# Optimization experiments

Measured on AMD Instinct MI355X. Metric: run time of the kernel, lower is better.

Reference implementation:

```python
import jax, jax.numpy as jnp
import numpy as np

D_MODEL = 1024
NUM_HEADS = 16
D_HEAD = D_MODEL // NUM_HEADS


def setup_inputs() -> dict:
    key = jax.random.key(0)
    ks = jax.random.split(key, 11)
    B, S = 2, 2048
    s = 1.0 / np.sqrt(D_MODEL)
    inp = {
        "Q": jax.random.normal(ks[0], (B, S, D_MODEL), dtype=jnp.float32),
        "K": jax.random.normal(ks[1], (B, S, D_MODEL), dtype=jnp.float32),
        "V": jax.random.normal(ks[2], (B, S, D_MODEL), dtype=jnp.float32),
        "W_q": jax.random.normal(ks[3], (D_MODEL, D_MODEL), dtype=jnp.float32) * s,
        "b_q": jnp.zeros((D_MODEL,), dtype=jnp.float32),
        "W_k": jax.random.normal(ks[4], (D_MODEL, D_MODEL), dtype=jnp.float32) * s,
        "b_k": jnp.zeros((D_MODEL,), dtype=jnp.float32),
        "W_v": jax.random.normal(ks[5], (D_MODEL, D_MODEL), dtype=jnp.float32) * s,
        "b_v": jnp.zeros((D_MODEL,), dtype=jnp.float32),
        "W_o": jax.random.normal(ks[6], (D_MODEL, D_MODEL), dtype=jnp.float32) * s,
        "b_o": jnp.zeros((D_MODEL,), dtype=jnp.float32),
    }
    return inp


def reference(Q, K, V, W_q, b_q, W_k, b_k, W_v, b_v, W_o, b_o):
    B, S, _ = Q.shape
    # Linear projections (torch Linear: x @ W.T + b)
    q = Q @ W_q.T + b_q  # [B,S,D]
    k = K @ W_k.T + b_k
    v = V @ W_v.T + b_v
    # split heads -> [B,H,S,d]
    q = q.reshape(B, S, NUM_HEADS, D_HEAD).transpose(0, 2, 1, 3)
    k = k.reshape(B, S, NUM_HEADS, D_HEAD).transpose(0, 2, 1, 3)
    v = v.reshape(B, S, NUM_HEADS, D_HEAD).transpose(0, 2, 1, 3)
    scores = jnp.einsum("bhqd,bhkd->bhqk", q, k) / np.sqrt(D_HEAD).astype(np.float32)
    attn = jax.nn.softmax(scores, axis=-1)
    out = jnp.einsum("bhqk,bhkd->bhqd", attn, v)
    out = out.transpose(0, 2, 1, 3).reshape(B, S, D_MODEL)
    return out @ W_o.T + b_o
```

## Files before the change

### kernel.cpp

```cpp
#include <hip/hip_runtime.h>
#include <stdint.h>

#define D_MODEL 1024
#define S_LEN   2048
#define BATCH   2
#define NHEAD   16
#define DHEAD   64
#define NTOK    (BATCH * S_LEN)

typedef unsigned short u16;
typedef __attribute__((ext_vector_type(8))) short bf16x8;
typedef __attribute__((ext_vector_type(4))) float f32x4;
typedef __attribute__((ext_vector_type(16))) float f32x16;
typedef __attribute__((ext_vector_type(2))) unsigned int u32x2;

__device__ __forceinline__ unsigned pack2bf(float lo, float hi) {
    unsigned a = __float_as_uint(lo) + 0x8000u;
    unsigned b = __float_as_uint(hi) + 0x8000u;
    return __builtin_amdgcn_perm(b, a, 0x07060302u);
}
__device__ __forceinline__ u16 f2bf1(float f) {
    return (u16)((__float_as_uint(f) + 0x8000u) >> 16);
}

#define GAS(p) ((const __attribute__((address_space(1))) void*)(p))
#define LAS(p) ((__attribute__((address_space(3))) void*)(p))
#define SWZ8(row, c) (((((row) << 3) | ((c) ^ ((row) & 7)))) << 3)

__global__ __launch_bounds__(256) void convert_kernel(
    const float* __restrict__ Q, const float* __restrict__ K, const float* __restrict__ V,
    const float* __restrict__ Wq, const float* __restrict__ Wk,
    const float* __restrict__ Wv, const float* __restrict__ Wo,
    u16* __restrict__ Qb, u16* __restrict__ Kb, u16* __restrict__ Vb,
    u16* __restrict__ Wqb, u16* __restrict__ Wkb, u16* __restrict__ Wvb, u16* __restrict__ Wob)
{
    const size_t SEG = 262144;
    size_t start = (size_t)blockIdx.x * 4096;
    int s = (int)(start / SEG);
    const float* src; u16* dst; size_t seg0;
    if (s < 4)       { src = Q;  dst = Qb;  seg0 = 0; }
    else if (s < 8)  { src = K;  dst = Kb;  seg0 = 4 * SEG; }
    else if (s < 12) { src = V;  dst = Vb;  seg0 = 8 * SEG; }
    else if (s == 12){ src = Wq; dst = Wqb; seg0 = 12 * SEG; }
    else if (s == 13){ src = Wk; dst = Wkb; seg0 = 13 * SEG; }
    else if (s == 14){ src = Wv; dst = Wvb; seg0 = 14 * SEG; }
    else             { src = Wo; dst = Wob; seg0 = 15 * SEG; }
    size_t off = start - seg0 + threadIdx.x;
    const float4* s4 = (const float4*)src;
    #pragma unroll
    for (int k = 0; k < 16; ++k) {
        float4 x = s4[off + (size_t)k * 256];
        u32x2 p = (u32x2){pack2bf(x.x, x.y), pack2bf(x.z, x.w)};
        *(u32x2*)(dst + (off + (size_t)k * 256) * 4) = p;
    }
}

__global__ __launch_bounds__(256) void proj_kernel(
    const u16* __restrict__ Qb, const u16* __restrict__ Kb, const u16* __restrict__ Vb,
    const u16* __restrict__ Wqb, const u16* __restrict__ Wkb, const u16* __restrict__ Wvb,
    const float* __restrict__ bq, const float* __restrict__ bk, const float* __restrict__ bv,
    u16* __restrict__ qw, u16* __restrict__ kw, u16* __restrict__ vtw)
{
    const int z = blockIdx.z;
    const int bx = blockIdx.x;
    const u16* A = (z == 0) ? Wqb : (z == 1) ? Wkb : Wvb;
    const u16* B = (z == 0) ? Qb  : (z == 1) ? Kb  : Vb;
    const float* bias = (z == 0) ? bq : (z == 1) ? bk : bv;
    const int mbase = (bx & 7) * 128;
    const int nbase = (bx >> 3) * 128;

    const int tid = threadIdx.x, lane = tid & 63, wave = tid >> 6;
    const int m16 = lane & 15, quad = lane >> 4;
    const int wm = wave >> 1, wn = wave & 1;

    __shared__ __align__(16) u16 As[128 * 64];
    __shared__ __align__(16) u16 Bs[128 * 64];

    int srow[4], scg[4];
    #pragma unroll
    for (int c = 0; c < 4; ++c) {
        int p = (wave * 4 + c) * 64 + lane;
        srow[c] = p >> 3;
        scg[c]  = (p & 7) ^ (srow[c] & 7);
    }

    f32x4 acc[4][4];
    #pragma unroll
    for (int mt = 0; mt < 4; ++mt)
        #pragma unroll
        for (int nt = 0; nt < 4; ++nt) acc[mt][nt] = (f32x4){0.f, 0.f, 0.f, 0.f};

    for (int kc = 0; kc < D_MODEL; kc += 64) {
        #pragma unroll
        for (int c = 0; c < 4; ++c) {
            __builtin_amdgcn_global_load_lds(
                GAS(A + (size_t)(mbase + srow[c]) * D_MODEL + kc + scg[c] * 8),
                LAS(As + (wave * 4 + c) * 512), 16, 0, 0);
            __builtin_amdgcn_global_load_lds(
                GAS(B + (size_t)(nbase + srow[c]) * D_MODEL + kc + scg[c] * 8),
                LAS(Bs + (wave * 4 + c) * 512), 16, 0, 0);
        }
        __syncthreads();
        #pragma unroll
        for (int half = 0; half < 2; ++half) {
            bf16x8 af[4], bfr[4];
            #pragma unroll
            for (int mt = 0; mt < 4; ++mt)
                af[mt] = *(const bf16x8*)&As[SWZ8(wm * 64 + mt * 16 + m16, quad + 4 * half)];
            #pragma unroll
            for (int nt = 0; nt < 4; ++nt)
                bfr[nt] = *(const bf16x8*)&Bs[SWZ8(wn * 64 + nt * 16 + m16, quad + 4 * half)];
            #pragma unroll
            for (int mt = 0; mt < 4; ++mt)
                #pragma unroll
                for (int nt = 0; nt < 4; ++nt)
                    acc[mt][nt] = __builtin_amdgcn_mfma_f32_16x16x32_bf16(af[mt], bfr[nt], acc[mt][nt], 0, 0, 0);
        }
        __syncthreads();
    }

    if (z < 2) {
        u16* Y = z ? kw : qw;
        const float scale = z ? 1.0f : 0.18033688011112042f;
        #pragma unroll
        for (int mt = 0; mt < 4; ++mt) {
            int d0 = mbase + wm * 64 + mt * 16 + quad * 4;
            float4 b4 = *(const float4*)&bias[d0];
            #pragma unroll
            for (int nt = 0; nt < 4; ++nt) {
                int tok = nbase + wn * 64 + nt * 16 + m16;
                float v0 = (acc[mt][nt][0] + b4.x) * scale;
                float v1 = (acc[mt][nt][1] + b4.y) * scale;
                float v2 = (acc[mt][nt][2] + b4.z) * scale;
                float v3 = (acc[mt][nt][3] + b4.w) * scale;
                *(u32x2*)(Y + (size_t)tok * D_MODEL + d0) =
                    (u32x2){pack2bf(v0, v1), pack2bf(v2, v3)};
            }
        }
    } else {
        #pragma unroll
        for (int mt = 0; mt < 4; ++mt)
            #pragma unroll
            for (int r = 0; r < 4; ++r) {
                int dout = mbase + wm * 64 + mt * 16 + quad * 4 + r;
                float bb = bias[dout];
                #pragma unroll
                for (int nt = 0; nt < 4; ++nt) {
                    int tok = nbase + wn * 64 + nt * 16 + m16;
                    vtw[(size_t)dout * NTOK + tok] = f2bf1(acc[mt][nt][r] + bb);
                }
            }
    }
}

__global__ __launch_bounds__(256, 2) void attn_kernel(
    const u16* __restrict__ qw, const u16* __restrict__ kw,
    const u16* __restrict__ vtw, u16* __restrict__ aw)
{
    const int qbase = blockIdx.x * 128;
    const int h = blockIdx.y, b = blockIdx.z;
    const int tid = threadIdx.x, lane = tid & 63, wave = tid >> 6;
    const int l31 = lane & 31;
    const int hh  = lane >> 5;
    const int colbase = h * DHEAD;
    const size_t qrow0 = (size_t)b * S_LEN + qbase;

    __shared__ __align__(16) u16 Ks[2][64 * 64];
    __shared__ __align__(16) u16 Vs[2][64 * 64];

    int srow[2], scg[2];
    #pragma unroll
    for (int i = 0; i < 2; ++i) {
        int p = (wave * 2 + i) * 64 + lane;
        srow[i] = p >> 3;
        scg[i]  = (p & 7) ^ (srow[i] & 7);
    }

    #define STAGE_KV(buf, kv0)                                                              \
        do {                                                                                \
            _Pragma("unroll")                                                               \
            for (int i_ = 0; i_ < 2; ++i_) {                                                \
                __builtin_amdgcn_global_load_lds(                                           \
                    GAS(kw + ((size_t)b * S_LEN + (kv0) + srow[i_]) * D_MODEL + colbase + scg[i_] * 8), \
                    LAS(Ks[buf] + (wave * 2 + i_) * 512), 16, 0, 0);                        \
                __builtin_amdgcn_global_load_lds(                                           \
                    GAS(vtw + (size_t)(colbase + srow[i_]) * NTOK + (size_t)b * S_LEN + (kv0) + scg[i_] * 8), \
                    LAS(Vs[buf] + (wave * 2 + i_) * 512), 16, 0, 0);                        \
            }                                                                               \
        } while (0)

    bf16x8 qf[4];
    {
        const u16* qptr = qw + (qrow0 + wave * 32 + l31) * D_MODEL + colbase + hh * 8;
        #pragma unroll
        for (int s = 0; s < 4; ++s) qf[s] = *(const bf16x8*)(qptr + s * 16);
    }

    STAGE_KV(0, 0);

    f32x16 o[2];
    #pragma unroll
    for (int dt = 0; dt < 2; ++dt)
        #pragma unroll
        for (int r = 0; r < 16; ++r) o[dt][r] = 0.f;
    float l = 0.f;

    __syncthreads();

    for (int t = 0; t < S_LEN / 64; ++t) {
        const int cur = t & 1;
        if (t + 1 < S_LEN / 64) STAGE_KV(!cur, (t + 1) * 64);

        f32x16 sc[2];
        #pragma unroll
        for (int kt = 0; kt < 2; ++kt) {
            #pragma unroll
            for (int r = 0; r < 16; ++r) sc[kt][r] = -12.f;
            #pragma unroll
            for (int s = 0; s < 4; ++s) {
                bf16x8 kf = *(const bf16x8*)&Ks[cur][SWZ8(kt * 32 + l31, s * 2 + hh)];
                sc[kt] = __builtin_amdgcn_mfma_f32_32x32x16_bf16(kf, qf[s], sc[kt], 0, 0, 0);
            }
        }

        unsigned x[2][4][2], y[2][4][2];
        #pragma unroll
        for (int kt = 0; kt < 2; ++kt)
            #pragma unroll
            for (int g = 0; g < 4; ++g) {
                float p0 = __builtin_amdgcn_exp2f(sc[kt][4 * g + 0]);
                float p1 = __builtin_amdgcn_exp2f(sc[kt][4 * g + 1]);
                float p2 = __builtin_amdgcn_exp2f(sc[kt][4 * g + 2]);
                float p3 = __builtin_amdgcn_exp2f(sc[kt][4 * g + 3]);
                l += (p0 + p1) + (p2 + p3);
                x[kt][g][0] = pack2bf(p0, p1);
                x[kt][g][1] = pack2bf(p2, p3);
            }
        #pragma unroll
        for (int kt = 0; kt < 2; ++kt)
            #pragma unroll
            for (int g = 0; g < 4; ++g) {
                y[kt][g][0] = __shfl_xor((int)x[kt][g][0], 32);
                y[kt][g][1] = __shfl_xor((int)x[kt][g][1], 32);
            }

        #pragma unroll
        for (int kt = 0; kt < 2; ++kt)
            #pragma unroll
            for (int sp = 0; sp < 2; ++sp) {
                int ge = 2 * sp, go = 2 * sp + 1;
                union { unsigned u[4]; bf16x8 v; } pf;
                pf.u[0] = hh ? y[kt][go][0] : x[kt][ge][0];
                pf.u[1] = hh ? y[kt][go][1] : x[kt][ge][1];
                pf.u[2] = hh ? x[kt][go][0] : y[kt][ge][0];
                pf.u[3] = hh ? x[kt][go][1] : y[kt][ge][1];
                #pragma unroll
                for (int dt = 0; dt < 2; ++dt) {
                    bf16x8 vf = *(const bf16x8*)&Vs[cur][SWZ8(dt * 32 + l31, (2 * kt + sp) * 2 + hh)];
                    o[dt] = __builtin_amdgcn_mfma_f32_32x32x16_bf16(vf, pf.v, o[dt], 0, 0, 0);
                }
            }

        __syncthreads();
    }

    l += __shfl_xor(l, 32);
    float inv = 1.0f / l;

    size_t orow = (qrow0 + wave * 32 + l31) * D_MODEL + colbase;
    #pragma unroll
    for (int dt = 0; dt < 2; ++dt)
        #pragma unroll
        for (int g = 0; g < 4; ++g) {
            float v0 = o[dt][4 * g + 0] * inv, v1 = o[dt][4 * g + 1] * inv;
            float v2 = o[dt][4 * g + 2] * inv, v3 = o[dt][4 * g + 3] * inv;
            *(u32x2*)(aw + orow + dt * 32 + 8 * g + 4 * hh) =
                (u32x2){pack2bf(v0, v1), pack2bf(v2, v3)};
        }
    #undef STAGE_KV
}

__global__ __launch_bounds__(256) void outproj_kernel(
    const u16* __restrict__ aw, const u16* __restrict__ Wob,
    const float* __restrict__ bo, float* __restrict__ out)
{
    const int nbase = blockIdx.x * 64;
    const int mbase = blockIdx.y * 128;
    const int tid = threadIdx.x, lane = tid & 63, wave = tid >> 6;
    const int m16 = lane & 15, quad = lane >> 4;
    const int wm = wave >> 1, wn = wave & 1;

    __shared__ __align__(16) u16 As[128 * 64];
    __shared__ __align__(16) u16 Bs[64 * 64];

    int arow[4], acg[4], brow[2], bcg[2];
    #pragma unroll
    for (int c = 0; c < 4; ++c) {
        int p = (wave * 4 + c) * 64 + lane;
        arow[c] = p >> 3; acg[c] = (p & 7) ^ (arow[c] & 7);
    }
    #pragma unroll
    for (int c = 0; c < 2; ++c) {
        int p = (wave * 2 + c) * 64 + lane;
        brow[c] = p >> 3; bcg[c] = (p & 7) ^ (brow[c] & 7);
    }

    f32x4 acc[4][2];
    #pragma unroll
    for (int mt = 0; mt < 4; ++mt)
        #pragma unroll
        for (int nt = 0; nt < 2; ++nt) acc[mt][nt] = (f32x4){0.f, 0.f, 0.f, 0.f};

    for (int kc = 0; kc < D_MODEL; kc += 64) {
        #pragma unroll
        for (int c = 0; c < 4; ++c)
            __builtin_amdgcn_global_load_lds(
                GAS(Wob + (size_t)(mbase + arow[c]) * D_MODEL + kc + acg[c] * 8),
                LAS(As + (wave * 4 + c) * 512), 16, 0, 0);
        #pragma unroll
        for (int c = 0; c < 2; ++c)
            __builtin_amdgcn_global_load_lds(
                GAS(aw + (size_t)(nbase + brow[c]) * D_MODEL + kc + bcg[c] * 8),
                LAS(Bs + (wave * 2 + c) * 512), 16, 0, 0);
        __syncthreads();
        #pragma unroll
        for (int half = 0; half < 2; ++half) {
            bf16x8 af[4], bfr[2];
            #pragma unroll
            for (int mt = 0; mt < 4; ++mt)
                af[mt] = *(const bf16x8*)&As[SWZ8(wm * 64 + mt * 16 + m16, quad + 4 * half)];
            #pragma unroll
            for (int nt = 0; nt < 2; ++nt)
                bfr[nt] = *(const bf16x8*)&Bs[SWZ8(wn * 32 + nt * 16 + m16, quad + 4 * half)];
            #pragma unroll
            for (int mt = 0; mt < 4; ++mt)
                #pragma unroll
                for (int nt = 0; nt < 2; ++nt)
                    acc[mt][nt] = __builtin_amdgcn_mfma_f32_16x16x32_bf16(af[mt], bfr[nt], acc[mt][nt], 0, 0, 0);
        }
        __syncthreads();
    }

    #pragma unroll
    for (int mt = 0; mt < 4; ++mt) {
        int d0 = mbase + wm * 64 + mt * 16 + quad * 4;
        float4 b4 = *(const float4*)&bo[d0];
        #pragma unroll
        for (int nt = 0; nt < 2; ++nt) {
            int tok = nbase + wn * 32 + nt * 16 + m16;
            float4 st;
            st.x = acc[mt][nt][0] + b4.x;
            st.y = acc[mt][nt][1] + b4.y;
            st.z = acc[mt][nt][2] + b4.z;
            st.w = acc[mt][nt][3] + b4.w;
            *(float4*)(out + (size_t)tok * D_MODEL + d0) = st;
        }
    }
}

extern "C" void kernel_launch(void* const* d_in, const int* in_sizes, int n_in,
                              void* d_out, int out_size, void* d_ws, size_t ws_size,
                              hipStream_t stream) {
    const float* Q  = (const float*)d_in[0];
    const float* K  = (const float*)d_in[1];
    const float* V  = (const float*)d_in[2];
    const float* Wq = (const float*)d_in[3];
    const float* bq = (const float*)d_in[4];
    const float* Wk = (const float*)d_in[5];
    const float* bk = (const float*)d_in[6];
    const float* Wv = (const float*)d_in[7];
    const float* bv = (const float*)d_in[8];
    const float* Wo = (const float*)d_in[9];
    const float* bo = (const float*)d_in[10];

    const size_t NT = (size_t)NTOK * D_MODEL;
    const size_t WN = (size_t)D_MODEL * D_MODEL;
    u16* base = (u16*)d_ws;
    u16* qw  = base;
    u16* kw  = base + NT;
    u16* vtw = base + 2 * NT;
    u16* Qb  = base + 3 * NT;
    u16* Kb  = base + 4 * NT;
    u16* Vb  = base + 5 * NT;
    u16* Wqb = base + 6 * NT;
    u16* Wkb = Wqb + WN;
    u16* Wvb = Wkb + WN;
    u16* Wob = Wvb + WN;
    u16* aww = Qb;

    convert_kernel<<<1024, 256, 0, stream>>>(Q, K, V, Wq, Wk, Wv, Wo,
                                             Qb, Kb, Vb, Wqb, Wkb, Wvb, Wob);
    proj_kernel<<<dim3(256, 1, 3), 256, 0, stream>>>(Qb, Kb, Vb, Wqb, Wkb, Wvb,
                                                     bq, bk, bv, qw, kw, vtw);
    attn_kernel<<<dim3(S_LEN / 128, NHEAD, BATCH), 256, 0, stream>>>(qw, kw, vtw, aww);
    outproj_kernel<<<dim3(NTOK / 64, D_MODEL / 128), 256, 0, stream>>>(
        aww, Wob, bo, (float*)d_out);
}
```

Before: 238.3 us.

## Split attention KV tiles across two wave groups with LDS reduction

The attention kernel now runs 512 threads per block. Each group of four waves processes one half of every 64-key tile, so each wave handles 32 keys instead of 64, and the two partial outputs and row sums are merged through shared memory at the end. The aim is more waves per CU to hide MFMA, exp and LDS latency, since the grid has only 512 blocks. The cost is a final LDS reduction pass, a larger shared-memory footprint and more waves contending at each tile barrier.

```diff
diff --git a/kernel.cpp b/kernel.cpp
--- a/kernel.cpp
+++ b/kernel.cpp
@@ -153,45 +153,40 @@
     }
 }
 
-__global__ __launch_bounds__(256, 2) void attn_kernel(
+__global__ __launch_bounds__(512, 4) void attn_kernel(
     const u16* __restrict__ qw, const u16* __restrict__ kw,
     const u16* __restrict__ vtw, u16* __restrict__ aw)
 {
     const int qbase = blockIdx.x * 128;
     const int h = blockIdx.y, b = blockIdx.z;
     const int tid = threadIdx.x, lane = tid & 63, wave = tid >> 6;
+    const int wq = wave & 3;
+    const int wk = wave >> 2;
     const int l31 = lane & 31;
     const int hh  = lane >> 5;
     const int colbase = h * DHEAD;
     const size_t qrow0 = (size_t)b * S_LEN + qbase;
 
-    __shared__ __align__(16) u16 Ks[2][64 * 64];
-    __shared__ __align__(16) u16 Vs[2][64 * 64];
-
-    int srow[2], scg[2];
-    #pragma unroll
-    for (int i = 0; i < 2; ++i) {
-        int p = (wave * 2 + i) * 64 + lane;
-        srow[i] = p >> 3;
-        scg[i]  = (p & 7) ^ (srow[i] & 7);
-    }
-
-    #define STAGE_KV(buf, kv0)                                                              \
-        do {                                                                                \
-            _Pragma("unroll")                                                               \
-            for (int i_ = 0; i_ < 2; ++i_) {                                                \
-                __builtin_amdgcn_global_load_lds(                                           \
-                    GAS(kw + ((size_t)b * S_LEN + (kv0) + srow[i_]) * D_MODEL + colbase + scg[i_] * 8), \
-                    LAS(Ks[buf] + (wave * 2 + i_) * 512), 16, 0, 0);                        \
-                __builtin_amdgcn_global_load_lds(                                           \
-                    GAS(vtw + (size_t)(colbase + srow[i_]) * NTOK + (size_t)b * S_LEN + (kv0) + scg[i_] * 8), \
-                    LAS(Vs[buf] + (wave * 2 + i_) * 512), 16, 0, 0);                        \
-            }                                                                               \
+    __shared__ __align__(16) u16 smem[17664];
+    #define KS_OFF(buf) ((buf) * 4096)
+    #define VS_OFF(buf) (8192 + (buf) * 4096)
+
+    const int srow = tid >> 3;
+    const int scg  = (tid & 7) ^ (srow & 7);
+    const size_t ksrc = ((size_t)b * S_LEN + srow) * D_MODEL + colbase + scg * 8;
+    const size_t vsrc = (size_t)(colbase + srow) * NTOK + (size_t)b * S_LEN + scg * 8;
+
+    #define STAGE_KV(buf, kv0)                                                         \
+        do {                                                                           \
+            __builtin_amdgcn_global_load_lds(GAS(kw + ksrc + (size_t)(kv0) * D_MODEL), \
+                                             LAS(smem + KS_OFF(buf) + wave * 512), 16, 0, 0); \
+            __builtin_amdgcn_global_load_lds(GAS(vtw + vsrc + (kv0)),                  \
+                                             LAS(smem + VS_OFF(buf) + wave * 512), 16, 0, 0); \
         } while (0)
 
     bf16x8 qf[4];
     {
-        const u16* qptr = qw + (qrow0 + wave * 32 + l31) * D_MODEL + colbase + hh * 8;
+        const u16* qptr = qw + (qrow0 + wq * 32 + l31) * D_MODEL + colbase + hh * 8;
         #pragma unroll
         for (int s = 0; s < 4; ++s) qf[s] = *(const bf16x8*)(qptr + s * 16);
     }
@@ -211,73 +206,85 @@
         const int cur = t & 1;
         if (t + 1 < S_LEN / 64) STAGE_KV(!cur, (t + 1) * 64);
 
-        f32x16 sc[2];
-        #pragma unroll
-        for (int kt = 0; kt < 2; ++kt) {
-            #pragma unroll
-            for (int r = 0; r < 16; ++r) sc[kt][r] = -12.f;
-            #pragma unroll
-            for (int s = 0; s < 4; ++s) {
-                bf16x8 kf = *(const bf16x8*)&Ks[cur][SWZ8(kt * 32 + l31, s * 2 + hh)];
-                sc[kt] = __builtin_amdgcn_mfma_f32_32x32x16_bf16(kf, qf[s], sc[kt], 0, 0, 0);
+        f32x16 sc;
+        #pragma unroll
+        for (int r = 0; r < 16; ++r) sc[r] = -12.f;
+        #pragma unroll
+        for (int s = 0; s < 4; ++s) {
+            bf16x8 kf = *(const bf16x8*)&smem[KS_OFF(cur) + SWZ8(wk * 32 + l31, s * 2 + hh)];
+            sc = __builtin_amdgcn_mfma_f32_32x32x16_bf16(kf, qf[s], sc, 0, 0, 0);
+        }
+
+        unsigned x[4][2], y[4][2];
+        #pragma unroll
+        for (int g = 0; g < 4; ++g) {
+            float p0 = __builtin_amdgcn_exp2f(sc[4 * g + 0]);
+            float p1 = __builtin_amdgcn_exp2f(sc[4 * g + 1]);
+            float p2 = __builtin_amdgcn_exp2f(sc[4 * g + 2]);
+            float p3 = __builtin_amdgcn_exp2f(sc[4 * g + 3]);
+            l += (p0 + p1) + (p2 + p3);
+            x[g][0] = pack2bf(p0, p1);
+            x[g][1] = pack2bf(p2, p3);
+        }
+        #pragma unroll
+        for (int g = 0; g < 4; ++g) {
+            y[g][0] = __shfl_xor((int)x[g][0], 32);
+            y[g][1] = __shfl_xor((int)x[g][1], 32);
+        }
+
+        #pragma unroll
+        for (int sp = 0; sp < 2; ++sp) {
+            const int ge = 2 * sp, go = 2 * sp + 1;
+            union { unsigned u[4]; bf16x8 v; } pf;
+            pf.u[0] = hh ? y[go][0] : x[ge][0];
+            pf.u[1] = hh ? y[go][1] : x[ge][1];
+            pf.u[2] = hh ? x[go][0] : y[ge][0];
+            pf.u[3] = hh ? x[go][1] : y[ge][1];
+            #pragma unroll
+            for (int dt = 0; dt < 2; ++dt) {
+                bf16x8 vf = *(const bf16x8*)&smem[VS_OFF(cur) + SWZ8(dt * 32 + l31, wk * 4 + sp * 2 + hh)];
+                o[dt] = __builtin_amdgcn_mfma_f32_32x32x16_bf16(vf, pf.v, o[dt], 0, 0, 0);
             }
         }
 
-        unsigned x[2][4][2], y[2][4][2];
-        #pragma unroll
-        for (int kt = 0; kt < 2; ++kt)
+        __syncthreads();
+    }
+
+    l += __shfl_xor(l, 32);
+
+    float* Ored = (float*)smem;
+    float* Lred = (float*)(smem + 17408);
+    float* op = Ored + ((size_t)wq * 32 + l31) * 68;
+    if (wk == 1) {
+        #pragma unroll
+        for (int dt = 0; dt < 2; ++dt)
+            #pragma unroll
+            for (int g = 0; g < 4; ++g)
+                *(f32x4*)(op + dt * 32 + 8 * g + 4 * hh) =
+                    (f32x4){o[dt][4 * g + 0], o[dt][4 * g + 1], o[dt][4 * g + 2], o[dt][4 * g + 3]};
+        if (hh == 0) Lred[wq * 32 + l31] = l;
+    }
+    __syncthreads();
+    if (wk == 0) {
+        l += Lred[wq * 32 + l31];
+        float inv = 1.0f / l;
+        size_t orow = (qrow0 + wq * 32 + l31) * D_MODEL + colbase;
+        #pragma unroll
+        for (int dt = 0; dt < 2; ++dt)
             #pragma unroll
             for (int g = 0; g < 4; ++g) {
-                float p0 = __builtin_amdgcn_exp2f(sc[kt][4 * g + 0]);
-                float p1 = __builtin_amdgcn_exp2f(sc[kt][4 * g + 1]);
-                float p2 = __builtin_amdgcn_exp2f(sc[kt][4 * g + 2]);
-                float p3 = __builtin_amdgcn_exp2f(sc[kt][4 * g + 3]);
-                l += (p0 + p1) + (p2 + p3);
-                x[kt][g][0] = pack2bf(p0, p1);
-                x[kt][g][1] = pack2bf(p2, p3);
+                f32x4 add = *(const f32x4*)(op + dt * 32 + 8 * g + 4 * hh);
+                float v0 = (o[dt][4 * g + 0] + add[0]) * inv;
+                float v1 = (o[dt][4 * g + 1] + add[1]) * inv;
+                float v2 = (o[dt][4 * g + 2] + add[2]) * inv;
+                float v3 = (o[dt][4 * g + 3] + add[3]) * inv;
+                *(u32x2*)(aw + orow + dt * 32 + 8 * g + 4 * hh) =
+                    (u32x2){pack2bf(v0, v1), pack2bf(v2, v3)};
             }
-        #pragma unroll
-        for (int kt = 0; kt < 2; ++kt)
-            #pragma unroll
-            for (int g = 0; g < 4; ++g) {
-                y[kt][g][0] = __shfl_xor((int)x[kt][g][0], 32);
-                y[kt][g][1] = __shfl_xor((int)x[kt][g][1], 32);
-            }
-
-        #pragma unroll
-        for (int kt = 0; kt < 2; ++kt)
-            #pragma unroll
-            for (int sp = 0; sp < 2; ++sp) {
-                int ge = 2 * sp, go = 2 * sp + 1;
-                union { unsigned u[4]; bf16x8 v; } pf;
-                pf.u[0] = hh ? y[kt][go][0] : x[kt][ge][0];
-                pf.u[1] = hh ? y[kt][go][1] : x[kt][ge][1];
-                pf.u[2] = hh ? x[kt][go][0] : y[kt][ge][0];
-                pf.u[3] = hh ? x[kt][go][1] : y[kt][ge][1];
-                #pragma unroll
-                for (int dt = 0; dt < 2; ++dt) {
-                    bf16x8 vf = *(const bf16x8*)&Vs[cur][SWZ8(dt * 32 + l31, (2 * kt + sp) * 2 + hh)];
-                    o[dt] = __builtin_amdgcn_mfma_f32_32x32x16_bf16(vf, pf.v, o[dt], 0, 0, 0);
-                }
-            }
-
-        __syncthreads();
-    }
-
-    l += __shfl_xor(l, 32);
-    float inv = 1.0f / l;
-
-    size_t orow = (qrow0 + wave * 32 + l31) * D_MODEL + colbase;
-    #pragma unroll
-    for (int dt = 0; dt < 2; ++dt)
-        #pragma unroll
-        for (int g = 0; g < 4; ++g) {
-            float v0 = o[dt][4 * g + 0] * inv, v1 = o[dt][4 * g + 1] * inv;
-            float v2 = o[dt][4 * g + 2] * inv, v3 = o[dt][4 * g + 3] * inv;
-            *(u32x2*)(aw + orow + dt * 32 + 8 * g + 4 * hh) =
-                (u32x2){pack2bf(v0, v1), pack2bf(v2, v3)};
-        }
+    }
     #undef STAGE_KV
+    #undef KS_OFF
+    #undef VS_OFF
 }
 
 __global__ __launch_bounds__(256) void outproj_kernel(
@@ -392,7 +399,7 @@
                                              Qb, Kb, Vb, Wqb, Wkb, Wvb, Wob);
     proj_kernel<<<dim3(256, 1, 3), 256, 0, stream>>>(Qb, Kb, Vb, Wqb, Wkb, Wvb,
                                                      bq, bk, bv, qw, kw, vtw);
-    attn_kernel<<<dim3(S_LEN / 128, NHEAD, BATCH), 256, 0, stream>>>(qw, kw, vtw, aww);
+    attn_kernel<<<dim3(S_LEN / 128, NHEAD, BATCH), 512, 0, stream>>>(qw, kw, vtw, aww);
     outproj_kernel<<<dim3(NTOK / 64, D_MODEL / 128), 256, 0, stream>>>(
         aww, Wob, bo, (float*)d_out);
 }
```

New measurement: 226.2 us. -5.1%, faster.
